# Kernel tuning notes

Hardware: AMD Instinct MI355X
Metric: run time of the kernel (lower is better)

## Reference

```python
import jax, jax.numpy as jnp
import numpy as np

R, E, A, F, K = 1024, 512, 128, 32, 31  # rnn_dim, embed_dim, attn_dim, n_filters, kernel
B, T = 64, 2048


def setup_inputs() -> dict:
    key = jax.random.key(0)
    ks = jax.random.split(key, 10)
    return {
        "attention_hidden": jax.random.normal(ks[0], (B, R), jnp.float32),
        "memory": jax.random.normal(ks[1], (B, T, E), jnp.float32),
        "attention_weights_cat": jax.random.uniform(ks[2], (B, 2, T), jnp.float32),
        "mask": jax.random.randint(ks[3], (B, T), 0, 2, jnp.int32),
        "W_query": jax.random.normal(ks[4], (R, A), jnp.float32) / np.sqrt(R),
        "W_memory": jax.random.normal(ks[5], (E, A), jnp.float32) / np.sqrt(E),
        "conv_w": jax.random.normal(ks[6], (F, 2, K), jnp.float32) / np.sqrt(2 * K),  # OIH
        "W_loc": jax.random.normal(ks[7], (F, A), jnp.float32) / np.sqrt(F),
        "v_w": jax.random.normal(ks[8], (A,), jnp.float32) / np.sqrt(A),
        "v_b": jax.random.normal(ks[9], (1,), jnp.float32) * 0.0,
    }


def reference(attention_hidden, memory, attention_weights_cat, mask,
              W_query, W_memory, conv_w, W_loc, v_w, v_b):
    # processed query: (B, A)
    pq = attention_hidden @ W_query
    # processed memory: (B, T, A)
    pm = jnp.einsum('bte,ea->bta', memory, W_memory)
    # location features: conv1d over (B, 2, T) with 'same' padding, no bias
    loc = jax.lax.conv_general_dilated(
        attention_weights_cat, conv_w,
        window_strides=(1,), padding=[((K - 1) // 2, (K - 1) // 2)],
        dimension_numbers=('NCH', 'OIH', 'NCH'))  # (B, F, T)
    pl = jnp.einsum('bft,fa->bta', loc, W_loc)  # (B, T, A)
    # energies: v(tanh(pm + pq + pl)) -> (B, T)
    energies = jnp.tanh(pm + pq[:, None, :] + pl) @ v_w + v_b[0]
    alignments = energies + mask.astype(energies.dtype) * -1e25
    attention_weights = jax.nn.softmax(alignments, axis=-1)
    # NOTE: original code (faithfully) uses raw alignments, not softmax weights
    attention_output = jnp.einsum('bt,bte->be', alignments, memory)
    return attention_output, attention_weights
```

## Files before the change

### kernel.cpp

```cpp
#include <hip/hip_runtime.h>

#define Bsz 64
#define Tsz 2048
#define Esz 512
#define Asz 128
#define Rsz 1024
#define KP  576
#define TILE_M 16

typedef __bf16 bf16;
typedef __bf16 bf16x8 __attribute__((ext_vector_type(8)));
typedef __bf16 bf16x4 __attribute__((ext_vector_type(4)));
typedef __bf16 bf16x2 __attribute__((ext_vector_type(2)));
typedef float  f32x4  __attribute__((ext_vector_type(4)));


__global__ __launch_bounds__(256) void prep_kernel(
    const float* __restrict__ Wmem, const float* __restrict__ convw,
    const float* __restrict__ Wloc, const float* __restrict__ ah,
    const float* __restrict__ Wq, bf16* __restrict__ Wext,
    float* __restrict__ pq)
{
  __shared__ f32x4 red[256];
  int blk = blockIdx.x, tid = threadIdx.x;
  if (blk < 128) {
    int a = blk;
    #pragma unroll
    for (int e = tid; e < Esz; e += 256)
      Wext[(size_t)(e >> 3)*(Asz*8) + a*8 + (e & 7)] = (bf16)Wmem[e*Asz + a];
  } else if (blk < 160) {
    int idx = (blk - 128)*256 + tid;
    int a = idx >> 6, j = idx & 63;
    float u = 0.f;
    if (j < 62) {
      int c  = (j < 31) ? 0 : 1;
      int kk = (j < 31) ? j : j - 31;
      #pragma unroll
      for (int f = 0; f < 32; ++f)
        u += convw[f*62 + c*31 + kk] * Wloc[f*Asz + a];
    }
    Wext[(size_t)(64 + (j >> 3))*(Asz*8) + a*8 + (j & 7)] = (bf16)u;
  } else {
    int b  = blk - 160;
    int cg = tid & 31;
    int kg = tid >> 5;
    const float* ahb = ah + (size_t)b*Rsz;
    f32x4 s = (f32x4){0.f,0.f,0.f,0.f};
    int r0 = kg*128;
    for (int r = r0; r < r0 + 128; ++r) {
      float av = ahb[r];
      f32x4 wq = *(const f32x4*)&Wq[r*Asz + cg*4];
      s += av * wq;
    }
    red[tid] = s;
    __syncthreads();
    if (tid < 32) {
      f32x4 tot = red[tid];
      #pragma unroll
      for (int g = 1; g < 8; ++g) tot += red[g*32 + tid];
      *(f32x4*)&pq[b*Asz + tid*4] = tot;
    }
  }
}

__device__ __forceinline__ float tanh_fast(float x) {
  float ex = __expf(2.f * x);
  return 1.f - 2.f / (ex + 1.f);
}

__global__ __launch_bounds__(256, 6) void attn_main(
    const float* __restrict__ memory, const float* __restrict__ awcat,
    const int* __restrict__ mask, const bf16* __restrict__ Wext,
    const float* __restrict__ pq, const float* __restrict__ vw,
    const float* __restrict__ vb, float* __restrict__ out,
    float* __restrict__ ws_align)
{
  __shared__ bf16  Afull[TILE_M * KP];
  __shared__ float s_pq[Asz];
  __shared__ float s_vw[Asz];
  __shared__ float s_ebuf[TILE_M];
  __shared__ float s_align[TILE_M];

  int tid = threadIdx.x;
  int b  = blockIdx.x >> 7;
  int t0 = (blockIdx.x & 127) << 4;

  const float4* memv = (const float4*)(memory + (size_t)(b*Tsz + t0)*Esz);
  #pragma unroll
  for (int p = 0; p < 8; ++p) {
    int i = tid + p*256;
    int r = i >> 7, c4 = i & 127;
    float4 v = memv[r*128 + c4];
    int k = c4 * 4;
    int sw = (k >> 3) ^ (r & 7);
    int base = r*KP + sw*8 + (k & 7);
    bf16x4 pk; pk[0]=(bf16)v.x; pk[1]=(bf16)v.y; pk[2]=(bf16)v.z; pk[3]=(bf16)v.w;
    *(bf16x4*)&Afull[base] = pk;
  }
  const float* aw = awcat + (size_t)b*2*Tsz;
  #pragma unroll
  for (int p = 0; p < 4; ++p) {
    int i = tid + p*256;
    int r = i >> 6, j = i & 63;
    float val = 0.f;
    if (j < 62) {
      int c  = (j < 31) ? 0 : 1;
      int kk = (j < 31) ? j : j - 31;
      int t  = t0 + r + kk - 15;
      if (t >= 0 && t < Tsz) val = aw[c*Tsz + t];
    }
    int k = Esz + j;
    int sw = (k >> 3) ^ (r & 7);
    Afull[r*KP + sw*8 + (k & 7)] = (bf16)val;
  }
  if (tid < Asz) { s_pq[tid] = pq[b*Asz + tid]; s_vw[tid] = vw[tid]; }
  if (tid < TILE_M) s_ebuf[tid] = 0.f;
  __syncthreads();

  int w = tid >> 6, l = tid & 63;
  int quad = l >> 4, lrow = l & 15;

  f32x4 acc[2];
  acc[0] = (f32x4){0.f, 0.f, 0.f, 0.f};
  acc[1] = (f32x4){0.f, 0.f, 0.f, 0.f};

  for (int kc = 0; kc < KP/32; ++kc) {
    int kg = kc*4 + quad;
    bf16x8 bfrag[2];
    #pragma unroll
    for (int nt = 0; nt < 2; ++nt) {
      int acol = lrow + 16*(2*w + nt);
      bfrag[nt] = *(const bf16x8*)&Wext[((size_t)kg*Asz + acol)*8];
    }
    bf16x8 afrag = *(const bf16x8*)&Afull[lrow*KP + ((kg ^ (lrow & 7)) << 3)];
    #pragma unroll
    for (int nt = 0; nt < 2; ++nt)
      acc[nt] = __builtin_amdgcn_mfma_f32_16x16x32_bf16(afrag, bfrag[nt], acc[nt], 0, 0, 0);
  }

  float partial[4];
  #pragma unroll
  for (int rg = 0; rg < 4; ++rg) partial[rg] = 0.f;
  #pragma unroll
  for (int nt = 0; nt < 2; ++nt) {
    int col = 16*(2*w + nt) + lrow;
    float vwc = s_vw[col], pqc = s_pq[col];
    #pragma unroll
    for (int rg = 0; rg < 4; ++rg)
      partial[rg] += tanh_fast(acc[nt][rg] + pqc) * vwc;
  }
  #pragma unroll
  for (int off = 1; off < 16; off <<= 1)
    #pragma unroll
    for (int rg = 0; rg < 4; ++rg)
      partial[rg] += __shfl_xor(partial[rg], off, 64);
  if (lrow == 0) {
    #pragma unroll
    for (int rg = 0; rg < 4; ++rg)
      atomicAdd(&s_ebuf[quad*4 + rg], partial[rg]);
  }
  __syncthreads();

  if (tid < TILE_M) {
    int t = t0 + tid;
    float al = s_ebuf[tid] + vb[0] + (float)mask[b*Tsz + t] * -1e25f;
    s_align[tid] = al;
    ws_align[b*Tsz + t] = al;
  }
  __syncthreads();

  int k0 = tid * 2;
  float a0 = 0.f, a1 = 0.f;
  #pragma unroll
  for (int r = 0; r < TILE_M; ++r) {
    float al = s_align[r];
    int sw = ((k0 >> 3) ^ (r & 7));
    bf16x2 m = *(const bf16x2*)&Afull[r*KP + sw*8 + (k0 & 7)];
    a0 += al * (float)m[0];
    a1 += al * (float)m[1];
  }
  atomicAdd(&out[b*Esz + k0],     a0);
  atomicAdd(&out[b*Esz + k0 + 1], a1);
}

__global__ __launch_bounds__(256) void softmax_kernel(
    const float* __restrict__ ws_align, float* __restrict__ out_w)
{
  int b = blockIdx.x, tid = threadIdx.x;
  const float* row = ws_align + (size_t)b*Tsz;
  float vals[8];
  float lmax = -3.4e38f;
  #pragma unroll
  for (int i = 0; i < 8; ++i) { vals[i] = row[tid + i*256]; lmax = fmaxf(lmax, vals[i]); }
  #pragma unroll
  for (int off = 1; off < 64; off <<= 1) lmax = fmaxf(lmax, __shfl_xor(lmax, off, 64));
  __shared__ float smax[4], ssum[4];
  if ((tid & 63) == 0) smax[tid >> 6] = lmax;
  __syncthreads();
  float bmax = fmaxf(fmaxf(smax[0], smax[1]), fmaxf(smax[2], smax[3]));
  float lsum = 0.f;
  #pragma unroll
  for (int i = 0; i < 8; ++i) { vals[i] = __expf(vals[i] - bmax); lsum += vals[i]; }
  #pragma unroll
  for (int off = 1; off < 64; off <<= 1) lsum += __shfl_xor(lsum, off, 64);
  if ((tid & 63) == 0) ssum[tid >> 6] = lsum;
  __syncthreads();
  float inv = 1.f / (ssum[0] + ssum[1] + ssum[2] + ssum[3]);
  #pragma unroll
  for (int i = 0; i < 8; ++i) out_w[(size_t)b*Tsz + tid + i*256] = vals[i] * inv;
}

extern "C" void kernel_launch(void* const* d_in, const int* in_sizes, int n_in,
                              void* d_out, int out_size, void* d_ws, size_t ws_size,
                              hipStream_t stream) {
  const float* ah   = (const float*)d_in[0];
  const float* mem  = (const float*)d_in[1];
  const float* awc  = (const float*)d_in[2];
  const int*   mask = (const int*)d_in[3];
  const float* Wq   = (const float*)d_in[4];
  const float* Wm   = (const float*)d_in[5];
  const float* cw   = (const float*)d_in[6];
  const float* Wl   = (const float*)d_in[7];
  const float* vw   = (const float*)d_in[8];
  const float* vb   = (const float*)d_in[9];
  float* out = (float*)d_out;

  bf16*  Wext = (bf16*)d_ws;
  float* pq   = (float*)((char*)d_ws + 147456);
  float* wsa  = (float*)((char*)d_ws + 180224);

  hipMemsetAsync(out, 0, Bsz*Esz*sizeof(float), stream);
  prep_kernel<<<dim3(224), 256, 0, stream>>>(Wm, cw, Wl, ah, Wq, Wext, pq);
  attn_main<<<dim3(Bsz*(Tsz/TILE_M)), 256, 0, stream>>>(mem, awc, mask, Wext, pq, vw, vb, out, wsa);
  softmax_kernel<<<dim3(Bsz), 256, 0, stream>>>(wsa, out + Bsz*Esz);
}
```

Measured before the change: 456.0 us.

## Double tile rows per block and replace global atomics with partial-sum reduction

```diff
diff --git a/kernel.cpp b/kernel.cpp
--- a/kernel.cpp
+++ b/kernel.cpp
@@ -6,7 +6,8 @@
 #define Asz 128
 #define Rsz 1024
 #define KP  576
-#define TILE_M 16
+#define TILE_M 32
+#define CHUNKS (Tsz / TILE_M)
 
 typedef __bf16 bf16;
 typedef __bf16 bf16x8 __attribute__((ext_vector_type(8)));
@@ -68,12 +69,13 @@
   return 1.f - 2.f / (ex + 1.f);
 }
 
-__global__ __launch_bounds__(256, 6) void attn_main(
+template<bool USE_POUT>
+__global__ __launch_bounds__(256, 4) void attn_main(
     const float* __restrict__ memory, const float* __restrict__ awcat,
     const int* __restrict__ mask, const bf16* __restrict__ Wext,
     const float* __restrict__ pq, const float* __restrict__ vw,
-    const float* __restrict__ vb, float* __restrict__ out,
-    float* __restrict__ ws_align)
+    const float* __restrict__ vb, float* __restrict__ pout,
+    float* __restrict__ outg, float* __restrict__ ws_align)
 {
   __shared__ bf16  Afull[TILE_M * KP];
   __shared__ float s_pq[Asz];
@@ -82,12 +84,12 @@
   __shared__ float s_align[TILE_M];
 
   int tid = threadIdx.x;
-  int b  = blockIdx.x >> 7;
-  int t0 = (blockIdx.x & 127) << 4;
+  int b  = blockIdx.x >> 6;
+  int t0 = (blockIdx.x & 63) << 5;
 
   const float4* memv = (const float4*)(memory + (size_t)(b*Tsz + t0)*Esz);
   #pragma unroll
-  for (int p = 0; p < 8; ++p) {
+  for (int p = 0; p < 16; ++p) {
     int i = tid + p*256;
     int r = i >> 7, c4 = i & 127;
     float4 v = memv[r*128 + c4];
@@ -99,7 +101,7 @@
   }
   const float* aw = awcat + (size_t)b*2*Tsz;
   #pragma unroll
-  for (int p = 0; p < 4; ++p) {
+  for (int p = 0; p < 8; ++p) {
     int i = tid + p*256;
     int r = i >> 6, j = i & 63;
     float val = 0.f;
@@ -120,44 +122,61 @@
   int w = tid >> 6, l = tid & 63;
   int quad = l >> 4, lrow = l & 15;
 
-  f32x4 acc[2];
-  acc[0] = (f32x4){0.f, 0.f, 0.f, 0.f};
-  acc[1] = (f32x4){0.f, 0.f, 0.f, 0.f};
+  f32x4 acc[2][2];
+  #pragma unroll
+  for (int mt = 0; mt < 2; ++mt)
+    #pragma unroll
+    for (int nt = 0; nt < 2; ++nt)
+      acc[mt][nt] = (f32x4){0.f, 0.f, 0.f, 0.f};
 
   for (int kc = 0; kc < KP/32; ++kc) {
     int kg = kc*4 + quad;
-    bf16x8 bfrag[2];
+    bf16x8 bfrag[2], afrag[2];
     #pragma unroll
     for (int nt = 0; nt < 2; ++nt) {
-      int acol = lrow + 16*(2*w + nt);
+      int acol = w*32 + nt*16 + lrow;
       bfrag[nt] = *(const bf16x8*)&Wext[((size_t)kg*Asz + acol)*8];
     }
-    bf16x8 afrag = *(const bf16x8*)&Afull[lrow*KP + ((kg ^ (lrow & 7)) << 3)];
-    #pragma unroll
-    for (int nt = 0; nt < 2; ++nt)
-      acc[nt] = __builtin_amdgcn_mfma_f32_16x16x32_bf16(afrag, bfrag[nt], acc[nt], 0, 0, 0);
-  }
-
-  float partial[4];
-  #pragma unroll
-  for (int rg = 0; rg < 4; ++rg) partial[rg] = 0.f;
+    #pragma unroll
+    for (int mt = 0; mt < 2; ++mt) {
+      int row = mt*16 + lrow;
+      afrag[mt] = *(const bf16x8*)&Afull[row*KP + ((kg ^ (row & 7)) << 3)];
+    }
+    #pragma unroll
+    for (int mt = 0; mt < 2; ++mt)
+      #pragma unroll
+      for (int nt = 0; nt < 2; ++nt)
+        acc[mt][nt] = __builtin_amdgcn_mfma_f32_16x16x32_bf16(afrag[mt], bfrag[nt], acc[mt][nt], 0, 0, 0);
+  }
+
+  float partial[2][4];
+  #pragma unroll
+  for (int mt = 0; mt < 2; ++mt)
+    #pragma unroll
+    for (int rg = 0; rg < 4; ++rg) partial[mt][rg] = 0.f;
   #pragma unroll
   for (int nt = 0; nt < 2; ++nt) {
-    int col = 16*(2*w + nt) + lrow;
+    int col = w*32 + nt*16 + lrow;
     float vwc = s_vw[col], pqc = s_pq[col];
     #pragma unroll
-    for (int rg = 0; rg < 4; ++rg)
-      partial[rg] += tanh_fast(acc[nt][rg] + pqc) * vwc;
+    for (int mt = 0; mt < 2; ++mt)
+      #pragma unroll
+      for (int rg = 0; rg < 4; ++rg)
+        partial[mt][rg] += tanh_fast(acc[mt][nt][rg] + pqc) * vwc;
   }
   #pragma unroll
   for (int off = 1; off < 16; off <<= 1)
     #pragma unroll
-    for (int rg = 0; rg < 4; ++rg)
-      partial[rg] += __shfl_xor(partial[rg], off, 64);
+    for (int mt = 0; mt < 2; ++mt)
+      #pragma unroll
+      for (int rg = 0; rg < 4; ++rg)
+        partial[mt][rg] += __shfl_xor(partial[mt][rg], off, 64);
   if (lrow == 0) {
     #pragma unroll
-    for (int rg = 0; rg < 4; ++rg)
-      atomicAdd(&s_ebuf[quad*4 + rg], partial[rg]);
+    for (int mt = 0; mt < 2; ++mt)
+      #pragma unroll
+      for (int rg = 0; rg < 4; ++rg)
+        atomicAdd(&s_ebuf[mt*16 + quad*4 + rg], partial[mt][rg]);
   }
   __syncthreads();
 
@@ -179,12 +198,19 @@
     a0 += al * (float)m[0];
     a1 += al * (float)m[1];
   }
-  atomicAdd(&out[b*Esz + k0],     a0);
-  atomicAdd(&out[b*Esz + k0 + 1], a1);
-}
-
+  if constexpr (USE_POUT) {
+    float2 o; o.x = a0; o.y = a1;
+    *(float2*)&pout[(size_t)blockIdx.x * Esz + k0] = o;
+  } else {
+    atomicAdd(&outg[b*Esz + k0],     a0);
+    atomicAdd(&outg[b*Esz + k0 + 1], a1);
+  }
+}
+
+template<bool REDUCE>
 __global__ __launch_bounds__(256) void softmax_kernel(
-    const float* __restrict__ ws_align, float* __restrict__ out_w)
+    const float* __restrict__ ws_align, const float* __restrict__ pout,
+    float* __restrict__ out_be, float* __restrict__ out_w)
 {
   int b = blockIdx.x, tid = threadIdx.x;
   const float* row = ws_align + (size_t)b*Tsz;
@@ -208,6 +234,17 @@
   float inv = 1.f / (ssum[0] + ssum[1] + ssum[2] + ssum[3]);
   #pragma unroll
   for (int i = 0; i < 8; ++i) out_w[(size_t)b*Tsz + tid + i*256] = vals[i] * inv;
+
+  if constexpr (REDUCE) {
+    float2 s; s.x = 0.f; s.y = 0.f;
+    const float2* pv = (const float2*)(pout + (size_t)b*CHUNKS*Esz) + tid;
+    #pragma unroll
+    for (int c = 0; c < CHUNKS; ++c) {
+      float2 v = pv[(size_t)c * (Esz/2)];
+      s.x += v.x; s.y += v.y;
+    }
+    *(float2*)&out_be[(size_t)b*Esz + tid*2] = s;
+  }
 }
 
 extern "C" void kernel_launch(void* const* d_in, const int* in_sizes, int n_in,
@@ -228,9 +265,19 @@
   bf16*  Wext = (bf16*)d_ws;
   float* pq   = (float*)((char*)d_ws + 147456);
   float* wsa  = (float*)((char*)d_ws + 180224);
-
-  hipMemsetAsync(out, 0, Bsz*Esz*sizeof(float), stream);
+  float* pout = (float*)((char*)d_ws + 180224 + (size_t)Bsz*Tsz*4);
+
+  size_t need = 180224 + (size_t)Bsz*Tsz*4 + (size_t)Bsz*CHUNKS*Esz*4;
+
   prep_kernel<<<dim3(224), 256, 0, stream>>>(Wm, cw, Wl, ah, Wq, Wext, pq);
-  attn_main<<<dim3(Bsz*(Tsz/TILE_M)), 256, 0, stream>>>(mem, awc, mask, Wext, pq, vw, vb, out, wsa);
-  softmax_kernel<<<dim3(Bsz), 256, 0, stream>>>(wsa, out + Bsz*Esz);
-}
+  if (ws_size >= need) {
+    attn_main<true><<<dim3(Bsz*CHUNKS), 256, 0, stream>>>(
+        mem, awc, mask, Wext, pq, vw, vb, pout, out, wsa);
+    softmax_kernel<true><<<dim3(Bsz), 256, 0, stream>>>(wsa, pout, out, out + Bsz*Esz);
+  } else {
+    hipMemsetAsync(out, 0, Bsz*Esz*sizeof(float), stream);
+    attn_main<false><<<dim3(Bsz*CHUNKS), 256, 0, stream>>>(
+        mem, awc, mask, Wext, pq, vw, vb, wsa , out, wsa);
+    softmax_kernel<false><<<dim3(Bsz), 256, 0, stream>>>(wsa, wsa, out, out + Bsz*Esz);
+  }
+}
```

Measured after the change: 449.3 us. Within noise of the previous version (-1.5%).
